# Performance work log

Measured on AMD Instinct MI355X. Metric: run time of the kernel, lower is better.

## Reference

```python
import jax, jax.numpy as jnp
import numpy as np

IN_FEATURES = 4096
OUT_FEATURES = 4096


def setup_inputs() -> dict:
    key = jax.random.key(0)
    k_x, k_w, k_b = jax.random.split(key, 3)
    inp = {
        "input": jax.random.normal(k_x, (4, 2048, IN_FEATURES), dtype=jnp.float32),
        # learned int8 weight table [out_features, in_features]
        "weight_int8": jax.random.randint(k_w, (OUT_FEATURES, IN_FEATURES), -128, 128, dtype=jnp.int32).astype(jnp.int8),
        # per-tensor dequant scales (scalars, as in the module buffers)
        "scale": jnp.asarray(0.01, dtype=jnp.float32),
        "x_scale": jnp.asarray(0.05, dtype=jnp.float32),
        "bias": jax.random.normal(k_b, (OUT_FEATURES,), dtype=jnp.float32) * 0.02,
    }
    return inp


def reference(input, weight_int8, scale, x_scale, bias):
    # --- quantize activations per-tensor to int8 (W8A8 path) ---
    x_int8 = jnp.clip(jnp.round(input / x_scale), -128, 127).astype(jnp.int8)
    in_shape = input.shape
    x_flat = x_int8.reshape(-1, in_shape[-1])  # [B*S, in]
    # contract x_flat[k] with weight_int8[n, k] -> [B*S, out]
    out_i32 = jax.lax.dot_general(
        x_flat, weight_int8,
        dimension_numbers=(((1,), (1,)), ((), ())),
        preferred_element_type=jnp.int32,
    )
    # --- dequant epilogue: combined scale, reshape, bias ---
    out = out_i32.astype(input.dtype) * (scale * x_scale)
    out = out.reshape(*in_shape[:-1], weight_int8.shape[0])
    out = out + bias
    return out
```

## Files before the change

kernel.cpp:

```cpp
#include <hip/hip_runtime.h>

#define KDIM 4096
#define NDIM 4096
#define BM 256
#define BN 256
#define BK 128
#define NTILE (KDIM / BK)

using i32x4 = __attribute__((ext_vector_type(4))) int;
using i32x16 = __attribute__((ext_vector_type(16))) int;

__device__ __forceinline__ void g2l16(const void* g, void* l) {
  __builtin_amdgcn_global_load_lds(
      (const __attribute__((address_space(1))) void*)g,
      (__attribute__((address_space(3))) void*)l,
      16, 0, 0);
}

__global__ void w8l_detect(const int* __restrict__ w32, int* __restrict__ flag) {
  __shared__ int s;
  const int t = threadIdx.x;
  if (t == 0) s = 1;
  __syncthreads();
  bool oob = false;
#pragma unroll
  for (int i = 0; i < 16; ++i) {
    int v = w32[t * 16 + i];
    if (v < -128 || v > 127) oob = true;
  }
  if (oob) atomicAnd(&s, 0);
  __syncthreads();
  if (t == 0) *flag = s;
}

__global__ void w8l_pack(const void* __restrict__ wsrc, const int* __restrict__ flag,
                         signed char* __restrict__ wq) {
  if (*flag == 0) return;
  const int t = blockIdx.x * blockDim.x + threadIdx.x;
  const int4* s = (const int4*)wsrc;
  int4 a = s[t * 4 + 0], b = s[t * 4 + 1], c = s[t * 4 + 2], d = s[t * 4 + 3];
  int4 o;
  o.x = (a.x & 255) | ((a.y & 255) << 8) | ((a.z & 255) << 16) | ((a.w & 255) << 24);
  o.y = (b.x & 255) | ((b.y & 255) << 8) | ((b.z & 255) << 16) | ((b.w & 255) << 24);
  o.z = (c.x & 255) | ((c.y & 255) << 8) | ((c.z & 255) << 16) | ((c.w & 255) << 24);
  o.w = (d.x & 255) | ((d.y & 255) << 8) | ((d.z & 255) << 16) | ((d.w & 255) << 24);
  ((int4*)wq)[t] = o;
}

__global__ void w8l_quant(const float* __restrict__ x, const float* __restrict__ xs,
                          signed char* __restrict__ xq) {
  const int t = blockIdx.x * blockDim.x + threadIdx.x;
  const float s = *xs;
  const float4* x4 = (const float4*)x;
  int4 o;
  int* op = (int*)&o;
#pragma unroll
  for (int q = 0; q < 4; ++q) {
    float4 f = x4[t * 4 + q];
    int v0 = __float2int_rn(f.x / s);
    int v1 = __float2int_rn(f.y / s);
    int v2 = __float2int_rn(f.z / s);
    int v3 = __float2int_rn(f.w / s);
    v0 = v0 < -128 ? -128 : (v0 > 127 ? 127 : v0);
    v1 = v1 < -128 ? -128 : (v1 > 127 ? 127 : v1);
    v2 = v2 < -128 ? -128 : (v2 > 127 ? 127 : v2);
    v3 = v3 < -128 ? -128 : (v3 > 127 ? 127 : v3);
    op[q] = (v0 & 255) | ((v1 & 255) << 8) | ((v2 & 255) << 16) | ((v3 & 255) << 24);
  }
  ((int4*)xq)[t] = o;
}

__global__ __launch_bounds__(512, 2) void w8l_gemm32(
    const signed char* __restrict__ Aq,
    const signed char* __restrict__ Wraw, const signed char* __restrict__ Wpk,
    const int* __restrict__ flag,
    const float* __restrict__ scale, const float* __restrict__ xscale,
    const float* __restrict__ bias, float* __restrict__ out, int nbn) {
  __shared__ signed char lds[131072];

  const signed char* __restrict__ Wq = (*flag) ? Wpk : Wraw;

  const int tid = threadIdx.x;
  const int lane = tid & 63;
  const int wid = tid >> 6;
  const int wr = wid >> 2;
  const int wc = wid & 3;
  const int l31 = lane & 31;
  const int l5 = lane >> 5;

  const int nwg = gridDim.x;
  const int cpx = nwg >> 3;
  const int bid = blockIdx.x;
  const int swz = (bid & 7) * cpx + (bid >> 3);
  const int bm = swz / nbn, bn = swz % nbn;
  const int m0 = bm * BM, n0 = bn * BN;

  const unsigned lin = (unsigned)tid * 16u;
  const unsigned r_in = lin >> 7;
  const unsigned c16 = (lin >> 4) & 7;
  const unsigned s_r = (r_in ^ (r_in >> 3)) & 7u;
  const unsigned swcol = ((c16 ^ s_r) << 4);
  const signed char* agp = Aq + (size_t)(m0 + r_in) * KDIM + swcol;
  const signed char* wgp = Wq + (size_t)(n0 + r_in) * KDIM + swcol;
  const unsigned ldsoff_thr = r_in * 128u + c16 * 16u;

#define ISSUE_TILE(t)                                                       \
  do {                                                                      \
    const int t_ = (t);                                                     \
    const size_t koff_ = (size_t)t_ * BK;                                   \
    signed char* lb_ = lds + (unsigned)(t_ & 1) * 65536u + ldsoff_thr;      \
    _Pragma("unroll") for (int u = 0; u < 4; ++u)                           \
      g2l16(agp + (size_t)(u * 64) * KDIM + koff_, lb_ + u * 8192);         \
    _Pragma("unroll") for (int u = 0; u < 4; ++u)                           \
      g2l16(wgp + (size_t)(u * 64) * KDIM + koff_, lb_ + 32768 + u * 8192); \
  } while (0)

#define RD_AB(av, bv, Ab, Bb, ks)                                            \
  do {                                                                       \
    _Pragma("unroll") for (int mi = 0; mi < 4; ++mi) {                       \
      const int r_ = wr * 128 + mi * 32 + l31;                               \
      const int sx_ = (r_ ^ (r_ >> 3)) & 7;                                  \
      av[mi] = *(const i32x4*)((Ab) + r_ * 128 +                             \
                               ((((ks) * 2 + l5) ^ sx_) << 4));              \
    }                                                                        \
    _Pragma("unroll") for (int nj = 0; nj < 2; ++nj) {                       \
      const int r_ = wc * 64 + nj * 32 + l31;                                \
      const int sx_ = (r_ ^ (r_ >> 3)) & 7;                                  \
      bv[nj] = *(const i32x4*)((Bb) + r_ * 128 +                             \
                               ((((ks) * 2 + l5) ^ sx_) << 4));              \
    }                                                                        \
  } while (0)

#define CLUSTER(av, bv)                                                      \
  __builtin_amdgcn_s_setprio(1);                                             \
  _Pragma("unroll") for (int mi = 0; mi < 4; ++mi)                           \
      _Pragma("unroll") for (int nj = 0; nj < 2; ++nj)                       \
          acc[mi][nj] = __builtin_amdgcn_mfma_i32_32x32x32_i8(               \
              av[mi], bv[nj], acc[mi][nj], 0, 0, 0);                         \
  __builtin_amdgcn_s_setprio(0);

#define WAIT_PREV6                                          \
  __builtin_amdgcn_sched_barrier(0);                        \
  asm volatile("s_waitcnt lgkmcnt(6)" ::: "memory");        \
  __builtin_amdgcn_sched_barrier(0);

  i32x16 acc[4][2] = {};
  i32x4 aE[4], bE[2], aO[4], bO[2];

  ISSUE_TILE(0);
  ISSUE_TILE(1);
  asm volatile("s_waitcnt vmcnt(8)" ::: "memory");
  __builtin_amdgcn_s_barrier();
  __builtin_amdgcn_sched_barrier(0);
  RD_AB(aE, bE, lds, lds + 32768, 0);
  __builtin_amdgcn_sched_barrier(0);

#pragma unroll 1
  for (int kt = 0; kt < NTILE; ++kt) {
    const signed char* Ab = lds + (kt & 1) * 65536;
    const signed char* Bb = Ab + 32768;

    RD_AB(aO, bO, Ab, Bb, 1);
    WAIT_PREV6;
    CLUSTER(aE, bE);
    __builtin_amdgcn_sched_barrier(0);
    RD_AB(aE, bE, Ab, Bb, 2);
    WAIT_PREV6;
    CLUSTER(aO, bO);
    __builtin_amdgcn_sched_barrier(0);
    RD_AB(aO, bO, Ab, Bb, 3);
    WAIT_PREV6;
    CLUSTER(aE, bE);
    __builtin_amdgcn_sched_barrier(0);
    asm volatile("s_waitcnt lgkmcnt(0)" ::: "memory");
    __builtin_amdgcn_sched_barrier(0);
    if (kt + 1 < NTILE) {
      asm volatile("s_waitcnt vmcnt(0)" ::: "memory");
      __builtin_amdgcn_s_barrier();
      __builtin_amdgcn_sched_barrier(0);
      if (kt + 2 < NTILE) ISSUE_TILE(kt + 2);
      const signed char* An = lds + ((kt + 1) & 1) * 65536;
      RD_AB(aE, bE, An, An + 32768, 0);
      __builtin_amdgcn_sched_barrier(0);
    }
    CLUSTER(aO, bO);
    __builtin_amdgcn_sched_barrier(0);
  }

  const float cs = scale[0] * xscale[0];
#pragma unroll
  for (int nj = 0; nj < 2; ++nj) {
    const int n = n0 + wc * 64 + nj * 32 + l31;
    const float bj = bias[n];
#pragma unroll
    for (int mi = 0; mi < 4; ++mi) {
      const int mbase = m0 + wr * 128 + mi * 32 + l5 * 4;
#pragma unroll
      for (int r = 0; r < 16; ++r) {
        const int m = mbase + (r & 3) + 8 * (r >> 2);
        out[(size_t)m * NDIM + n] = (float)acc[mi][nj][r] * cs + bj;
      }
    }
  }
#undef ISSUE_TILE
#undef RD_AB
#undef CLUSTER
#undef WAIT_PREV6
}

extern "C" void kernel_launch(void* const* d_in, const int* in_sizes, int n_in,
                              void* d_out, int out_size, void* d_ws, size_t ws_size,
                              hipStream_t stream) {
  const float* x = (const float*)d_in[0];
  const void* w = d_in[1];
  const float* scale = (const float*)d_in[2];
  const float* xscale = (const float*)d_in[3];
  const float* bias = (const float*)d_in[4];
  float* out = (float*)d_out;

  const int M = in_sizes[0] / KDIM;

  int* flag = (int*)d_ws;
  signed char* wq = (signed char*)d_ws + 256;
  signed char* aq = wq + (size_t)NDIM * KDIM;

  const size_t need = 256 + (size_t)NDIM * KDIM + (size_t)M * KDIM;
  if (ws_size < need) return;

  w8l_detect<<<1, 256, 0, stream>>>((const int*)w, flag);
  w8l_pack<<<(NDIM * KDIM / 16) / 256, 256, 0, stream>>>(w, flag, wq);
  w8l_quant<<<(M * KDIM / 16) / 256, 256, 0, stream>>>(x, xscale, aq);

  const int nbn = NDIM / BN;
  w8l_gemm32<<<(M / BM) * nbn, 512, 0, stream>>>(
      aq, (const signed char*)w, wq, flag, scale, xscale, bias, out, nbn);
}
```

Baseline: 194.6 us.

## Restructure GEMM main loop into barrier-synchronized four-phase schedule with split A/B prefetch

Replaces the two-tile-ahead prefetch and double-buffered register fragments with a single fragment set and a one-tile-ahead prefetch. The A and B loads for the next k-tile are issued in separate phases, and s_barriers surround every MFMA group so the waves run in lockstep. The aim is to interleave global-to-LDS traffic with MFMA work more evenly and cut register pressure. In exchange it adds many workgroup barriers, shortens how far ahead data is fetched, and waits on vmcnt(0) within each tile, which may expose memory latency.

```diff
diff --git a/kernel.cpp b/kernel.cpp
--- a/kernel.cpp
+++ b/kernel.cpp
@@ -70,7 +70,7 @@
   ((int4*)xq)[t] = o;
 }
 
-__global__ __launch_bounds__(512, 2) void w8l_gemm32(
+__global__ __launch_bounds__(512, 2) void w8l_gemm(
     const signed char* __restrict__ Aq,
     const signed char* __restrict__ Wraw, const signed char* __restrict__ Wpk,
     const int* __restrict__ flag,
@@ -95,96 +95,108 @@
   const int bm = swz / nbn, bn = swz % nbn;
   const int m0 = bm * BM, n0 = bn * BN;
 
-  const unsigned lin = (unsigned)tid * 16u;
-  const unsigned r_in = lin >> 7;
-  const unsigned c16 = (lin >> 4) & 7;
+  const unsigned r_in = (unsigned)tid >> 3;
+  const unsigned c16 = (unsigned)tid & 7;
   const unsigned s_r = (r_in ^ (r_in >> 3)) & 7u;
   const unsigned swcol = ((c16 ^ s_r) << 4);
   const signed char* agp = Aq + (size_t)(m0 + r_in) * KDIM + swcol;
   const signed char* wgp = Wq + (size_t)(n0 + r_in) * KDIM + swcol;
-  const unsigned ldsoff_thr = r_in * 128u + c16 * 16u;
-
-#define ISSUE_TILE(t)                                                       \
-  do {                                                                      \
-    const int t_ = (t);                                                     \
-    const size_t koff_ = (size_t)t_ * BK;                                   \
-    signed char* lb_ = lds + (unsigned)(t_ & 1) * 65536u + ldsoff_thr;      \
-    _Pragma("unroll") for (int u = 0; u < 4; ++u)                           \
-      g2l16(agp + (size_t)(u * 64) * KDIM + koff_, lb_ + u * 8192);         \
-    _Pragma("unroll") for (int u = 0; u < 4; ++u)                           \
-      g2l16(wgp + (size_t)(u * 64) * KDIM + koff_, lb_ + 32768 + u * 8192); \
+  const unsigned ldsoff = (unsigned)tid * 16u;
+
+#define ISSUE_A(t)                                                           \
+  do {                                                                       \
+    const size_t koff_ = (size_t)(t) * BK;                                   \
+    signed char* lb_ = lds + (unsigned)((t) & 1) * 65536u + ldsoff;          \
+    _Pragma("unroll") for (int u = 0; u < 4; ++u)                            \
+      g2l16(agp + (size_t)(u * 64) * KDIM + koff_, lb_ + u * 8192);          \
   } while (0)
-
-#define RD_AB(av, bv, Ab, Bb, ks)                                            \
+#define ISSUE_B(t)                                                           \
+  do {                                                                       \
+    const size_t koff_ = (size_t)(t) * BK;                                   \
+    signed char* lb_ = lds + (unsigned)((t) & 1) * 65536u + 32768u + ldsoff; \
+    _Pragma("unroll") for (int u = 0; u < 4; ++u)                            \
+      g2l16(wgp + (size_t)(u * 64) * KDIM + koff_, lb_ + u * 8192);          \
+  } while (0)
+
+#define RD(base, ks)                                                         \
   do {                                                                       \
     _Pragma("unroll") for (int mi = 0; mi < 4; ++mi) {                       \
       const int r_ = wr * 128 + mi * 32 + l31;                               \
       const int sx_ = (r_ ^ (r_ >> 3)) & 7;                                  \
-      av[mi] = *(const i32x4*)((Ab) + r_ * 128 +                             \
+      af[mi] = *(const i32x4*)((base) + r_ * 128 +                           \
                                ((((ks) * 2 + l5) ^ sx_) << 4));              \
     }                                                                        \
     _Pragma("unroll") for (int nj = 0; nj < 2; ++nj) {                       \
       const int r_ = wc * 64 + nj * 32 + l31;                                \
       const int sx_ = (r_ ^ (r_ >> 3)) & 7;                                  \
-      bv[nj] = *(const i32x4*)((Bb) + r_ * 128 +                             \
+      bf[nj] = *(const i32x4*)((base) + 32768 + r_ * 128 +                   \
                                ((((ks) * 2 + l5) ^ sx_) << 4));              \
     }                                                                        \
   } while (0)
 
-#define CLUSTER(av, bv)                                                      \
+#define SB __builtin_amdgcn_sched_barrier(0)
+
+#define MFMA8                                                                \
   __builtin_amdgcn_s_setprio(1);                                             \
   _Pragma("unroll") for (int mi = 0; mi < 4; ++mi)                           \
       _Pragma("unroll") for (int nj = 0; nj < 2; ++nj)                       \
           acc[mi][nj] = __builtin_amdgcn_mfma_i32_32x32x32_i8(               \
-              av[mi], bv[nj], acc[mi][nj], 0, 0, 0);                         \
+              af[mi], bf[nj], acc[mi][nj], 0, 0, 0);                         \
   __builtin_amdgcn_s_setprio(0);
 
-#define WAIT_PREV6                                          \
-  __builtin_amdgcn_sched_barrier(0);                        \
-  asm volatile("s_waitcnt lgkmcnt(6)" ::: "memory");        \
-  __builtin_amdgcn_sched_barrier(0);
-
   i32x16 acc[4][2] = {};
-  i32x4 aE[4], bE[2], aO[4], bO[2];
-
-  ISSUE_TILE(0);
-  ISSUE_TILE(1);
-  asm volatile("s_waitcnt vmcnt(8)" ::: "memory");
+  i32x4 af[4], bf[2];
+
+  ISSUE_A(0);
+  ISSUE_B(0);
+  asm volatile("s_waitcnt vmcnt(0)" ::: "memory");
   __builtin_amdgcn_s_barrier();
-  __builtin_amdgcn_sched_barrier(0);
-  RD_AB(aE, bE, lds, lds + 32768, 0);
-  __builtin_amdgcn_sched_barrier(0);
+  SB;
 
 #pragma unroll 1
   for (int kt = 0; kt < NTILE; ++kt) {
-    const signed char* Ab = lds + (kt & 1) * 65536;
-    const signed char* Bb = Ab + 32768;
-
-    RD_AB(aO, bO, Ab, Bb, 1);
-    WAIT_PREV6;
-    CLUSTER(aE, bE);
-    __builtin_amdgcn_sched_barrier(0);
-    RD_AB(aE, bE, Ab, Bb, 2);
-    WAIT_PREV6;
-    CLUSTER(aO, bO);
-    __builtin_amdgcn_sched_barrier(0);
-    RD_AB(aO, bO, Ab, Bb, 3);
-    WAIT_PREV6;
-    CLUSTER(aE, bE);
-    __builtin_amdgcn_sched_barrier(0);
-    asm volatile("s_waitcnt lgkmcnt(0)" ::: "memory");
-    __builtin_amdgcn_sched_barrier(0);
-    if (kt + 1 < NTILE) {
-      asm volatile("s_waitcnt vmcnt(0)" ::: "memory");
-      __builtin_amdgcn_s_barrier();
-      __builtin_amdgcn_sched_barrier(0);
-      if (kt + 2 < NTILE) ISSUE_TILE(kt + 2);
-      const signed char* An = lds + ((kt + 1) & 1) * 65536;
-      RD_AB(aE, bE, An, An + 32768, 0);
-      __builtin_amdgcn_sched_barrier(0);
-    }
-    CLUSTER(aO, bO);
-    __builtin_amdgcn_sched_barrier(0);
+    const signed char* base = lds + (unsigned)(kt & 1) * 65536u;
+
+    RD(base, 0);
+    SB;
+    if (kt + 1 < NTILE) ISSUE_A(kt + 1);
+    SB;
+    __builtin_amdgcn_s_barrier();
+    asm volatile("s_waitcnt lgkmcnt(0)" ::: "memory");
+    SB;
+    MFMA8;
+    SB;
+    __builtin_amdgcn_s_barrier();
+
+    RD(base, 1);
+    SB;
+    if (kt + 1 < NTILE) ISSUE_B(kt + 1);
+    SB;
+    __builtin_amdgcn_s_barrier();
+    asm volatile("s_waitcnt lgkmcnt(0)" ::: "memory");
+    SB;
+    MFMA8;
+    SB;
+    __builtin_amdgcn_s_barrier();
+
+    RD(base, 2);
+    SB;
+    __builtin_amdgcn_s_barrier();
+    asm volatile("s_waitcnt lgkmcnt(0)" ::: "memory");
+    SB;
+    MFMA8;
+    SB;
+    __builtin_amdgcn_s_barrier();
+
+    RD(base, 3);
+    SB;
+    asm volatile("s_waitcnt vmcnt(0)" ::: "memory");
+    __builtin_amdgcn_s_barrier();
+    asm volatile("s_waitcnt lgkmcnt(0)" ::: "memory");
+    SB;
+    MFMA8;
+    SB;
+    __builtin_amdgcn_s_barrier();
   }
 
   const float cs = scale[0] * xscale[0];
@@ -202,10 +214,11 @@
       }
     }
   }
-#undef ISSUE_TILE
-#undef RD_AB
-#undef CLUSTER
-#undef WAIT_PREV6
+#undef ISSUE_A
+#undef ISSUE_B
+#undef RD
+#undef MFMA8
+#undef SB
 }
 
 extern "C" void kernel_launch(void* const* d_in, const int* in_sizes, int n_in,
@@ -232,6 +245,6 @@
   w8l_quant<<<(M * KDIM / 16) / 256, 256, 0, stream>>>(x, xscale, aq);
 
   const int nbn = NDIM / BN;
-  w8l_gemm32<<<(M / BM) * nbn, 512, 0, stream>>>(
+  w8l_gemm<<<(M / BM) * nbn, 512, 0, stream>>>(
       aq, (const signed char*)w, wq, flag, scale, xscale, bias, out, nbn);
 }
```

New measurement: 199.0 us. +2.3%, slower.
